# Performance work log

Hardware: AMD Instinct MI355X
Metric: run time of the kernel (lower is better)

Reference implementation:

```python
import jax, jax.numpy as jnp
import numpy as np

H, D, R, S, K, EV = 8, 256, 6, 2, 2, 2   # num_heads, head_dim, ratio, shared_head, topk, expand_v
HID = 2048
DV = D * EV            # head_v_dim = 512
KEY_DIM = H * D        # 2048
VAL_DIM = KEY_DIM * EV # 4096


def setup_inputs() -> dict:
    key = jax.random.key(0)
    ks = jax.random.split(key, 9)
    b, t = 2, 1024
    def lin(k, fan_in, shape):
        # ~torch default linear init scale
        return jax.random.normal(k, shape, jnp.float32) * (fan_in ** -0.5)
    return {
        "hidden_states": jax.random.normal(ks[0], (b, t, HID), jnp.float32),
        "Wq": lin(ks[1], HID, (HID, KEY_DIM)),
        "Wk": lin(ks[2], HID, (HID, KEY_DIM)),
        "Wv": lin(ks[3], HID, (HID, VAL_DIM)),
        "Wq_exp": lin(ks[4], D, (H, D, D * R)),  # per-head q expert expansion (ModuleList -> batched)
        "Wk_exp": lin(ks[5], D, (H, D, D * R)),
        "Wgate": lin(ks[6], D, (D, R - S)),
        "Wg": lin(ks[7], HID, (HID, VAL_DIM)),
        "Wo": lin(ks[8], VAL_DIM, (VAL_DIM, HID)),
    }


def reference(hidden_states, Wq, Wk, Wv, Wq_exp, Wk_exp, Wgate, Wg, Wo):
    b, t, _ = hidden_states.shape
    # base projections, split into heads: [H, b, t, D]
    q = (hidden_states @ Wq).reshape(b, t, H, D).transpose(2, 0, 1, 3)
    k = (hidden_states @ Wk).reshape(b, t, H, D).transpose(2, 0, 1, 3)
    v = (hidden_states @ Wv).reshape(b, t, H, DV)  # [b, t, H, DV]

    # --- sparse routing on q (gate over ratio - shared experts) ---
    logits = jnp.einsum('hbtd,dn->hbtn', q, Wgate)
    scores = jax.nn.softmax(logits.astype(jnp.float32), axis=-1)
    w, idx = jax.lax.top_k(scores, K)
    w = w / jnp.sum(w, axis=-1, keepdims=True)
    idx = idx + S  # shift past shared experts
    # scatter top-k weights into full [H, b, t, R]
    full = jnp.sum(jax.nn.one_hot(idx, R, dtype=w.dtype) * w[..., None], axis=-2)
    full = full.at[..., :S].set(1.0 / S)
    full = full / jnp.sum(full, axis=-1, keepdims=True)
    rw = full.astype(hidden_states.dtype).transpose(3, 1, 2, 0)  # [R, b, t, H]
    mask = (rw != 0).astype(hidden_states.dtype)                 # [R, b, t, H]

    # --- per-head expert expansions: [R, b, t, H, D] ---
    qe = jnp.einsum('hbtd,hde->hbte', q, Wq_exp).reshape(H, b, t, R, D).transpose(3, 1, 2, 0, 4)
    ke = jnp.einsum('hbtd,hde->hbte', k, Wk_exp).reshape(H, b, t, R, D).transpose(3, 1, 2, 0, 4)
    ve = jnp.broadcast_to(v[None], (R, b, t, H, DV))
    qe = qe * mask[..., None]
    ke = ke * mask[..., None]
    ve = ve * mask[..., None]

    # --- dense attention per (expert, batch, head) ---
    attn = jax.nn.softmax(jnp.einsum('rbqhd,rbkhd->rbhqk', qe, ke) / (D ** 0.5), axis=-1)
    o = jnp.einsum('rbhqk,rbkhd->rbqhd', attn, ve)  # [R, b, t, H, DV]

    # --- weighted combine over experts + gated output ---
    o = jnp.einsum('rbthd,rbth->bthd', o, rw)
    g = (hidden_states @ Wg).reshape(b, t, H, DV)
    o = o * jax.nn.silu(g)
    return o.reshape(b, t, VAL_DIM) @ Wo
```

## Files before the change

### kernel.cpp

```cpp
#include <hip/hip_runtime.h>
#include <hip/hip_bf16.h>
#include <cstdint>
#include <cstddef>

typedef __bf16 bf16_t;
typedef __bf16 bf16x8 __attribute__((ext_vector_type(8)));
typedef float f32x4 __attribute__((ext_vector_type(4)));

typedef __attribute__((address_space(3))) unsigned int lds_uint_t;
typedef __attribute__((address_space(1))) unsigned int glob_uint_t;

__device__ __forceinline__ void gload16(const void* g, void* l) {
  __builtin_amdgcn_global_load_lds((const glob_uint_t*)g, (lds_uint_t*)l, 16, 0, 0);
}

__device__ __forceinline__ f32x4 mfma16(bf16x8 a, bf16x8 b, f32x4 c) {
  return __builtin_amdgcn_mfma_f32_16x16x32_bf16(a, b, c, 0, 0, 0);
}

__global__ __launch_bounds__(256) void conv_bf16_k(const float* __restrict__ in,
                                                   bf16_t* __restrict__ out, int n8) {
  int i = blockIdx.x * 256 + threadIdx.x;
  if (i >= n8) return;
  f32x4 a = *(const f32x4*)(in + (size_t)i * 8);
  f32x4 b = *(const f32x4*)(in + (size_t)i * 8 + 4);
  bf16x8 o;
  o[0] = (bf16_t)a[0]; o[1] = (bf16_t)a[1]; o[2] = (bf16_t)a[2]; o[3] = (bf16_t)a[3];
  o[4] = (bf16_t)b[0]; o[5] = (bf16_t)b[1]; o[6] = (bf16_t)b[2]; o[7] = (bf16_t)b[3];
  *(bf16x8*)(out + (size_t)i * 8) = o;
}

__global__ __launch_bounds__(256) void tconv_k(const float* __restrict__ in, bf16_t* __restrict__ out,
                                               int R, int C, size_t inZ, size_t outZ) {
  __shared__ __align__(16) bf16_t t[64 * 72];
  in += (size_t)blockIdx.z * inZ;
  out += (size_t)blockIdx.z * outZ;
  const int c0 = blockIdx.x * 64, r0 = blockIdx.y * 64;
  const int tid = threadIdx.x;
#pragma unroll
  for (int it = 0; it < 4; it++) {
    int c = tid + it * 256;
    int row = c >> 4, ch = c & 15;
    f32x4 v = *(const f32x4*)(in + (size_t)(r0 + row) * C + c0 + ch * 4);
#pragma unroll
    for (int j = 0; j < 4; j++) t[(ch * 4 + j) * 72 + row] = (bf16_t)v[j];
  }
  __syncthreads();
#pragma unroll
  for (int it = 0; it < 2; it++) {
    int c = tid + it * 256;
    int oc = c >> 3, ch = c & 7;
    bf16x8 v = *(const bf16x8*)(t + oc * 72 + ch * 8);
    *(bf16x8*)(out + (size_t)(c0 + oc) * R + r0 + ch * 8) = v;
  }
}

__global__ __launch_bounds__(256) void tv_k(const bf16_t* __restrict__ v, bf16_t* __restrict__ Vt) {
  __shared__ __align__(16) bf16_t t[64 * 72];
  const int tt0 = blockIdx.x * 64;
  const int dv0 = blockIdx.y * 64;
  const int bh = blockIdx.z;
  const int b = bh >> 3, h = bh & 7;
  const int tid = threadIdx.x;
  const bf16_t* src = v + (size_t)(b * 1024 + tt0) * 12288 + 8192 + h * 512 + dv0;
#pragma unroll
  for (int it = 0; it < 2; it++) {
    int c = tid + it * 256;
    int row = c >> 3, ch = c & 7;
    bf16x8 x = *(const bf16x8*)(src + (size_t)row * 12288 + ch * 8);
#pragma unroll
    for (int j = 0; j < 8; j++) t[(ch * 8 + j) * 72 + row] = x[j];
  }
  __syncthreads();
  bf16_t* dst = Vt + (size_t)bh * 524288 + (size_t)dv0 * 1024 + tt0;
#pragma unroll
  for (int it = 0; it < 2; it++) {
    int c = tid + it * 256;
    int od = c >> 3, ch = c & 7;
    bf16x8 x = *(const bf16x8*)(t + od * 72 + ch * 8);
    *(bf16x8*)(dst + (size_t)od * 1024 + ch * 8) = x;
  }
}

__global__ __launch_bounds__(256) void wfuse_k(const float* __restrict__ Wq, const float* __restrict__ Wgate,
                                               float* __restrict__ Wf) {
  __shared__ float wg[1024];
  const int tid = threadIdx.x;
  for (int i = tid; i < 1024; i += 256) wg[i] = Wgate[i];
  __syncthreads();
  const int kk = blockIdx.x * 64 + (tid & 63);
  const int oid = tid >> 6;
  float acc[8] = {0, 0, 0, 0, 0, 0, 0, 0};
  const float* wr = Wq + (size_t)kk * 2048;
#pragma unroll
  for (int half = 0; half < 2; half++) {
    const int h = oid * 2 + half;
    const float* seg = wr + h * 256;
    for (int d = 0; d < 256; d += 4) {
      f32x4 q4 = *(const f32x4*)(seg + d);
#pragma unroll
      for (int n = 0; n < 4; n++) {
        acc[half * 4 + n] += q4[0] * wg[(d + 0) * 4 + n] + q4[1] * wg[(d + 1) * 4 + n] +
                             q4[2] * wg[(d + 2) * 4 + n] + q4[3] * wg[(d + 3) * 4 + n];
      }
    }
  }
#pragma unroll
  for (int jj = 0; jj < 8; jj++) Wf[(size_t)kk * 32 + oid * 8 + jj] = acc[jj];
}

__global__ __launch_bounds__(256) void logits_k(const float* __restrict__ hs, const float* __restrict__ Wf,
                                                float* __restrict__ lg) {
  __shared__ __align__(16) float hrow[2048];
  __shared__ float red[8][32];
  const int bt = blockIdx.x;
  const int tid = threadIdx.x;
  const float* src = hs + (size_t)bt * 2048;
  for (int i = tid; i < 512; i += 256) *(f32x4*)&hrow[i * 4] = *(const f32x4*)(src + i * 4);
  __syncthreads();
  const int j = tid & 31, part = tid >> 5;
  float acc = 0.f;
  for (int kk = part * 256; kk < part * 256 + 256; kk++) acc += hrow[kk] * Wf[(size_t)kk * 32 + j];
  red[part][j] = acc;
  __syncthreads();
  if (tid < 32) {
    float s = 0.f;
#pragma unroll
    for (int p = 0; p < 8; p++) s += red[p][tid];
    lg[(size_t)bt * 32 + tid] = s;
  }
}

__global__ __launch_bounds__(256) void routing_k(const float* __restrict__ lg, float* __restrict__ rw) {
  int gid = blockIdx.x * 256 + threadIdx.x;
  if (gid >= 16384) return;
  const int h = gid >> 11;
  const int bt = gid & 2047;
  const int b = bt >> 10, tt = bt & 1023;
  f32x4 l = *(const f32x4*)(lg + (size_t)bt * 32 + h * 4);
  float mx = fmaxf(fmaxf(l[0], l[1]), fmaxf(l[2], l[3]));
  float e0 = __expf(l[0] - mx), e1 = __expf(l[1] - mx), e2 = __expf(l[2] - mx), e3 = __expf(l[3] - mx);
  float den = e0 + e1 + e2 + e3;
  float s[4] = {e0 / den, e1 / den, e2 / den, e3 / den};
  int i1 = 0;
#pragma unroll
  for (int i = 1; i < 4; i++) if (s[i] > s[i1]) i1 = i;
  int i2 = (i1 == 0) ? 1 : 0;
#pragma unroll
  for (int i = 0; i < 4; i++) if (i != i1 && s[i] > s[i2]) i2 = i;
  float sw = s[i1] + s[i2];
  float w1 = s[i1] / sw, w2 = s[i2] / sw;
  float tot = 1.0f + w1 + w2;
  float o[6] = {0.5f / tot, 0.5f / tot, 0.f, 0.f, 0.f, 0.f};
  o[2 + i1] = w1 / tot;
  o[2 + i2] = w2 / tot;
#pragma unroll
  for (int r = 0; r < 6; r++) rw[(size_t)((r * 2 + b) * 8 + h) * 1024 + tt] = o[r];
}

template <int MODE>
__global__ __launch_bounds__(256) void gemm_bt(const bf16_t* __restrict__ A, const bf16_t* __restrict__ B,
                                               void* __restrict__ Cp, int K, int lda, int ldb, int ldc) {
  __shared__ __align__(16) bf16_t lsA[128 * 64];
  __shared__ __align__(16) bf16_t lsB[128 * 64];
  const int tid = threadIdx.x;
  const int lane = tid & 63, wv = tid >> 6;
  const int lrow = lane & 15, lgrp = lane >> 4;
  const int wr = wv >> 1, wc = wv & 1;
  const int bn = blockIdx.x * 128, bm = blockIdx.y * 128;

  f32x4 zero = {0.f, 0.f, 0.f, 0.f};
  f32x4 acc[4][4];
#pragma unroll
  for (int i = 0; i < 4; i++)
#pragma unroll
    for (int j = 0; j < 4; j++) acc[i][j] = zero;

  for (int k0 = 0; k0 < K; k0 += 64) {
    __syncthreads();
#pragma unroll
    for (int it = 0; it < 4; it++) {
      int c = tid + it * 256;
      int row = c >> 3, coff = (c & 7) * 16;
      gload16((const char*)A + ((size_t)(bm + row) * lda + k0) * 2 + coff, (char*)lsA + row * 128 + coff);
      gload16((const char*)B + ((size_t)(bn + row) * ldb + k0) * 2 + coff, (char*)lsB + row * 128 + coff);
    }
    __syncthreads();
#pragma unroll
    for (int kk = 0; kk < 2; kk++) {
      bf16x8 af[4], bfr[4];
#pragma unroll
      for (int m4 = 0; m4 < 4; m4++)
        af[m4] = *(const bf16x8*)((const char*)lsA + (wr * 64 + m4 * 16 + lrow) * 128 + kk * 64 + lgrp * 16);
#pragma unroll
      for (int n4 = 0; n4 < 4; n4++)
        bfr[n4] = *(const bf16x8*)((const char*)lsB + (wc * 64 + n4 * 16 + lrow) * 128 + kk * 64 + lgrp * 16);
#pragma unroll
      for (int m4 = 0; m4 < 4; m4++)
#pragma unroll
        for (int n4 = 0; n4 < 4; n4++) acc[m4][n4] = mfma16(af[m4], bfr[n4], acc[m4][n4]);
    }
  }
#pragma unroll
  for (int m4 = 0; m4 < 4; m4++) {
#pragma unroll
    for (int i = 0; i < 4; i++) {
      const int row = bm + wr * 64 + m4 * 16 + lgrp * 4 + i;
#pragma unroll
      for (int n4 = 0; n4 < 4; n4++) {
        const int col = bn + wc * 64 + n4 * 16 + lrow;
        float v = acc[m4][n4][i];
        if constexpr (MODE == 0) {
          ((bf16_t*)Cp)[(size_t)row * ldc + col] = (bf16_t)v;
        } else {
          ((float*)Cp)[(size_t)row * ldc + col] = v;
        }
      }
    }
  }
}

__global__ __launch_bounds__(256) void gemm_exp(const bf16_t* __restrict__ qkg, const bf16_t* __restrict__ Wqe,
                                                const bf16_t* __restrict__ Wke, bf16_t* __restrict__ qeB,
                                                bf16_t* __restrict__ keB) {
  __shared__ __align__(16) bf16_t lsA[128 * 64];
  __shared__ __align__(16) bf16_t lsB[128 * 64];
  const int tid = threadIdx.x;
  const int lane = tid & 63, wv = tid >> 6;
  const int lrow = lane & 15, lgrp = lane >> 4;
  const int wr = wv >> 1, wc = wv & 1;
  const int bn = blockIdx.x * 128, bm = blockIdx.y * 128;
  const int z = blockIdx.z;
  const int sel = z >> 3, hh = z & 7;
  const bf16_t* A = qkg + sel * 2048 + hh * 256;
  const bf16_t* B = (sel ? Wke : Wqe) + (size_t)hh * 393216;
  bf16_t* C = sel ? keB : qeB;

  f32x4 zero = {0.f, 0.f, 0.f, 0.f};
  f32x4 acc[4][4];
#pragma unroll
  for (int i = 0; i < 4; i++)
#pragma unroll
    for (int j = 0; j < 4; j++) acc[i][j] = zero;

  for (int k0 = 0; k0 < 256; k0 += 64) {
    __syncthreads();
#pragma unroll
    for (int it = 0; it < 4; it++) {
      int c = tid + it * 256;
      int row = c >> 3, coff = (c & 7) * 16;
      gload16((const char*)A + ((size_t)(bm + row) * 12288 + k0) * 2 + coff, (char*)lsA + row * 128 + coff);
      gload16((const char*)B + ((size_t)(bn + row) * 256 + k0) * 2 + coff, (char*)lsB + row * 128 + coff);
    }
    __syncthreads();
#pragma unroll
    for (int kk = 0; kk < 2; kk++) {
      bf16x8 af[4], bfr[4];
#pragma unroll
      for (int m4 = 0; m4 < 4; m4++)
        af[m4] = *(const bf16x8*)((const char*)lsA + (wr * 64 + m4 * 16 + lrow) * 128 + kk * 64 + lgrp * 16);
#pragma unroll
      for (int n4 = 0; n4 < 4; n4++)
        bfr[n4] = *(const bf16x8*)((const char*)lsB + (wc * 64 + n4 * 16 + lrow) * 128 + kk * 64 + lgrp * 16);
#pragma unroll
      for (int m4 = 0; m4 < 4; m4++)
#pragma unroll
        for (int n4 = 0; n4 < 4; n4++) acc[m4][n4] = mfma16(af[m4], bfr[n4], acc[m4][n4]);
    }
  }
#pragma unroll
  for (int m4 = 0; m4 < 4; m4++) {
#pragma unroll
    for (int i = 0; i < 4; i++) {
      const int row = bm + wr * 64 + m4 * 16 + lgrp * 4 + i;
      const int bb = row >> 10, tt = row & 1023;
#pragma unroll
      for (int n4 = 0; n4 < 4; n4++) {
        const int col = bn + wc * 64 + n4 * 16 + lrow;
        const int rr = col >> 8, dd = col & 255;
        C[((size_t)((rr * 2 + bb) * 8 + hh) * 1024 + tt) * 256 + dd] = (bf16_t)acc[m4][n4][i];
      }
    }
  }
}

__global__ __launch_bounds__(256, 2) void attn_k(const bf16_t* __restrict__ qe, const bf16_t* __restrict__ ke,
                                                 const bf16_t* __restrict__ Vt, const float* __restrict__ rw,
                                                 const bf16_t* __restrict__ g, bf16_t* __restrict__ oc) {
  __shared__ __align__(16) bf16_t ldsK[2][32 * 256];
  __shared__ __align__(16) bf16_t ldsV[2][256 * 32];
  __shared__ __align__(16) bf16_t ldsP[4 * 16 * 40];

  const int f = (blockIdx.x & 7) * 64 + (blockIdx.x >> 3);
  const int qt = f & 15, dvh = (f >> 4) & 1, bh = f >> 5;

  const int tid = threadIdx.x;
  const int wv = tid >> 6, lane = tid & 63;
  const int lrow = lane & 15, lgrp = lane >> 4;
  const int b = bh >> 3, h = bh & 7;
  const int qw = qt * 64 + wv * 16;

  const char* vbase = (const char*)Vt + ((size_t)bh * 524288 + (size_t)dvh * 262144) * 2;

  auto issue_tile = [&](int rr, int kt, int buf) {
    const char* kb = (const char*)ke + ((size_t)((rr * 2 + b) * 8 + h) * 262144 + (size_t)kt * 8192) * 2;
    char* lk = (char*)ldsK[buf];
#pragma unroll
    for (int it = 0; it < 4; it++) {
      int p = (wv * 4 + it) * 1024 + (lane << 4);
      int row = p >> 9, off = p & 511;
      gload16(kb + (size_t)row * 512 + (off ^ ((row & 7) << 4)), lk + p);
    }
    const char* vb = vbase + kt * 64;
    char* lv = (char*)ldsV[buf];
#pragma unroll
    for (int it = 0; it < 4; it++) {
      int p = (wv * 4 + it) * 1024 + (lane << 4);
      int row = p >> 6, off = p & 63;
      gload16(vb + (size_t)row * 2048 + (off ^ (((row >> 1) & 3) << 4)), lv + p);
    }
  };

  f32x4 zero = {0.f, 0.f, 0.f, 0.f};
  f32x4 Otot[16];
#pragma unroll
  for (int n = 0; n < 16; n++) Otot[n] = zero;

  int cur = 0;
  issue_tile(0, 0, 0);

  for (int r = 0; r < 6; r++) {
    const size_t rbh = (size_t)((r * 2 + b) * 8 + h);
    const bf16_t* qbase = qe + rbh * 262144;
    const float* rwb = rw + rbh * 1024;

    bf16x8 qf[8];
#pragma unroll
    for (int c = 0; c < 8; c++)
      qf[c] = *(const bf16x8*)(qbase + (size_t)(qw + lrow) * 256 + c * 32 + lgrp * 8);
    float rwq[4];
#pragma unroll
    for (int i = 0; i < 4; i++) rwq[i] = rwb[qw + lgrp * 4 + i];

    float Lp[4] = {0.f, 0.f, 0.f, 0.f};
    f32x4 accO[16];
#pragma unroll
    for (int n = 0; n < 16; n++) accO[n] = zero;

    for (int kt = 0; kt < 32; kt++) {
      asm volatile("s_waitcnt vmcnt(0) lgkmcnt(0)" ::: "memory");
      __syncthreads();
      {
        int nr = r + ((kt == 31) ? 1 : 0);
        int nkt = (kt + 1) & 31;
        if (nr < 6) issue_tile(nr, nkt, cur ^ 1);
      }
      const char* lK = (const char*)ldsK[cur];
      const char* lV = (const char*)ldsV[cur];
      const float* rwk = rwb + kt * 32;
      float mk0 = rwk[lrow], mk1 = rwk[16 + lrow];

      f32x4 sac0 = zero, sac1 = zero;
      __builtin_amdgcn_s_setprio(1);
#pragma unroll
      for (int c = 0; c < 8; c++) {
        int col = (c * 64 + lgrp * 16) ^ ((lrow & 7) << 4);
        bf16x8 k0 = *(const bf16x8*)(lK + (size_t)lrow * 512 + col);
        bf16x8 k1 = *(const bf16x8*)(lK + (size_t)(16 + lrow) * 512 + col);
        sac0 = mfma16(qf[c], k0, sac0);
        sac1 = mfma16(qf[c], k1, sac1);
      }
      __builtin_amdgcn_s_setprio(0);
      bf16_t* pb = ldsP + wv * 640;
#pragma unroll
      for (int i = 0; i < 4; i++) {
        float e0 = __expf(sac0[i] * 0.0625f);
        float e1 = __expf(sac1[i] * 0.0625f);
        pb[(i * 4 + lgrp) * 40 + lrow] = (bf16_t)((mk0 != 0.f) ? e0 : 0.f);
        pb[(i * 4 + lgrp) * 40 + 16 + lrow] = (bf16_t)((mk1 != 0.f) ? e1 : 0.f);
        Lp[i] += ((mk0 != 0.f) ? e0 : 1.f) + ((mk1 != 0.f) ? e1 : 1.f);
      }
      bf16x8 pa = *(const bf16x8*)(pb + ((lrow & 3) * 4 + (lrow >> 2)) * 40 + lgrp * 8);
      __builtin_amdgcn_s_setprio(1);
#pragma unroll
      for (int n = 0; n < 16; n++) {
        int row = n * 16 + lrow;
        int col = (lgrp * 16) ^ (((row >> 1) & 3) << 4);
        bf16x8 vf = *(const bf16x8*)(lV + (size_t)row * 64 + col);
        accO[n] = mfma16(pa, vf, accO[n]);
      }
      __builtin_amdgcn_s_setprio(0);
      cur ^= 1;
    }
#pragma unroll
    for (int i = 0; i < 4; i++) {
      float v = Lp[i];
      v += __shfl_xor(v, 1, 16);
      v += __shfl_xor(v, 2, 16);
      v += __shfl_xor(v, 4, 16);
      v += __shfl_xor(v, 8, 16);
      float inv = rwq[i] / v;
#pragma unroll
      for (int n = 0; n < 16; n++) Otot[n][i] += accO[n][i] * inv;
    }
  }

#pragma unroll
  for (int i = 0; i < 4; i++) {
    const size_t grow = ((size_t)(b * 1024 + qw + lgrp * 4 + i)) * 12288 + 4096 + h * 512 + dvh * 256;
    const size_t orow = ((size_t)(b * 1024 + qw + lgrp * 4 + i)) * 4096 + h * 512 + dvh * 256;
#pragma unroll
    for (int n = 0; n < 16; n++) {
      float gv = (float)g[grow + n * 16 + lrow];
      float sg = gv / (1.f + __expf(-gv));
      oc[orow + n * 16 + lrow] = (bf16_t)(Otot[n][i] * sg);
    }
  }
}

extern "C" void kernel_launch(void* const* d_in, const int* in_sizes, int n_in,
                              void* d_out, int out_size, void* d_ws, size_t ws_size,
                              hipStream_t stream) {
  const float* hs  = (const float*)d_in[0];
  const float* Wq  = (const float*)d_in[1];
  const float* Wk  = (const float*)d_in[2];
  const float* Wv  = (const float*)d_in[3];
  const float* Wqe = (const float*)d_in[4];
  const float* Wke = (const float*)d_in[5];
  const float* Wgt = (const float*)d_in[6];
  const float* Wg  = (const float*)d_in[7];
  const float* Wo  = (const float*)d_in[8];
  float* out = (float*)d_out;

  const size_t MB = 1024 * 1024;
  char* w = (char*)d_ws;
  bf16_t* hs_bf = (bf16_t*)(w + 0 * MB);
  bf16_t* WcatT = (bf16_t*)(w + 8 * MB);
  bf16_t* qeB   = (bf16_t*)(w + 0 * MB);
  bf16_t* WoT   = (bf16_t*)(w + 56 * MB);
  bf16_t* WqeT  = (bf16_t*)(w + 72 * MB);
  bf16_t* WkeT  = (bf16_t*)(w + 78 * MB);
  bf16_t* qkg   = (bf16_t*)(w + 84 * MB);
  bf16_t* Vt    = (bf16_t*)(w + 132 * MB);
  bf16_t* keB   = (bf16_t*)(w + 148 * MB);
  bf16_t* ocB   = (bf16_t*)(w + 196 * MB);
  float*  Wf    = (float*)(w + 212 * MB);
  float*  lg    = (float*)(w + 212 * MB + 262144);
  float*  rwB   = (float*)(w + 212 * MB + 524288);
  (void)ws_size; (void)in_sizes; (void)n_in; (void)out_size;

  conv_bf16_k<<<2048, 256, 0, stream>>>(hs, hs_bf, 524288);
  tconv_k<<<dim3(32, 32, 1), 256, 0, stream>>>(Wq, WcatT, 2048, 2048, 0, 0);
  tconv_k<<<dim3(32, 32, 1), 256, 0, stream>>>(Wk, WcatT + 2048 * 2048, 2048, 2048, 0, 0);
  tconv_k<<<dim3(64, 32, 1), 256, 0, stream>>>(Wg, WcatT + 4096 * 2048, 2048, 4096, 0, 0);
  tconv_k<<<dim3(64, 32, 1), 256, 0, stream>>>(Wv, WcatT + 8192 * 2048, 2048, 4096, 0, 0);
  tconv_k<<<dim3(32, 64, 1), 256, 0, stream>>>(Wo, WoT, 4096, 2048, 0, 0);
  tconv_k<<<dim3(24, 4, 8), 256, 0, stream>>>(Wqe, WqeT, 256, 1536, 393216, 393216);
  tconv_k<<<dim3(24, 4, 8), 256, 0, stream>>>(Wke, WkeT, 256, 1536, 393216, 393216);

  wfuse_k<<<32, 256, 0, stream>>>(Wq, Wgt, Wf);
  logits_k<<<2048, 256, 0, stream>>>(hs, Wf, lg);
  routing_k<<<64, 256, 0, stream>>>(lg, rwB);

  gemm_bt<0><<<dim3(96, 16, 1), 256, 0, stream>>>(hs_bf, WcatT, qkg, 2048, 2048, 2048, 12288);
  tv_k<<<dim3(16, 8, 16), 256, 0, stream>>>(qkg, Vt);

  gemm_exp<<<dim3(12, 16, 16), 256, 0, stream>>>(qkg, WqeT, WkeT, qeB, keB);

  attn_k<<<512, 256, 0, stream>>>(qeB, keB, Vt, rwB, qkg, ocB);

  gemm_bt<2><<<dim3(16, 16, 1), 256, 0, stream>>>(ocB, WoT, out, 4096, 4096, 4096, 2048);
}
```

Measured before the change: 723.3 us.

## Shrink attention blocks to two waves, single-buffer tiles, add N64 output GEMM

The attention kernel moves from 4-wave blocks over 64 queries to 2-wave blocks over 32 queries, launching twice as many blocks. It also drops K/V double buffering in favour of a single LDS buffer with synchronous load, wait and sync on every tile. The output projection now uses a new 128x64-tile GEMM instead of the 128x128 one, giving more blocks for better CU coverage. The costs are more K/V reloads from global memory per query, no overlap of loads with MFMA work, and an extra barrier per iteration.

```diff
diff --git a/kernel.cpp b/kernel.cpp
--- a/kernel.cpp
+++ b/kernel.cpp
@@ -220,6 +220,65 @@
   }
 }
 
+__global__ __launch_bounds__(256) void gemm_n64(const bf16_t* __restrict__ A, const bf16_t* __restrict__ B,
+                                                float* __restrict__ C, int K, int lda, int ldb, int ldc) {
+  __shared__ __align__(16) bf16_t lsA[128 * 64];
+  __shared__ __align__(16) bf16_t lsB[64 * 64];
+  const int tid = threadIdx.x;
+  const int lane = tid & 63, wr = tid >> 6;
+  const int lrow = lane & 15, lgrp = lane >> 4;
+  const int bn = blockIdx.x * 64, bm = blockIdx.y * 128;
+
+  f32x4 zero = {0.f, 0.f, 0.f, 0.f};
+  f32x4 acc[2][4];
+#pragma unroll
+  for (int i = 0; i < 2; i++)
+#pragma unroll
+    for (int j = 0; j < 4; j++) acc[i][j] = zero;
+
+  for (int k0 = 0; k0 < K; k0 += 64) {
+    __syncthreads();
+#pragma unroll
+    for (int it = 0; it < 4; it++) {
+      int c = tid + it * 256;
+      int row = c >> 3, coff = (c & 7) * 16;
+      gload16((const char*)A + ((size_t)(bm + row) * lda + k0) * 2 + coff, (char*)lsA + row * 128 + coff);
+    }
+#pragma unroll
+    for (int it = 0; it < 2; it++) {
+      int c = tid + it * 256;
+      int row = c >> 3, coff = (c & 7) * 16;
+      gload16((const char*)B + ((size_t)(bn + row) * ldb + k0) * 2 + coff, (char*)lsB + row * 128 + coff);
+    }
+    __syncthreads();
+#pragma unroll
+    for (int kk = 0; kk < 2; kk++) {
+      bf16x8 af[2], bfr[4];
+#pragma unroll
+      for (int m2 = 0; m2 < 2; m2++)
+        af[m2] = *(const bf16x8*)((const char*)lsA + (wr * 32 + m2 * 16 + lrow) * 128 + kk * 64 + lgrp * 16);
+#pragma unroll
+      for (int n4 = 0; n4 < 4; n4++)
+        bfr[n4] = *(const bf16x8*)((const char*)lsB + (n4 * 16 + lrow) * 128 + kk * 64 + lgrp * 16);
+#pragma unroll
+      for (int m2 = 0; m2 < 2; m2++)
+#pragma unroll
+        for (int n4 = 0; n4 < 4; n4++) acc[m2][n4] = mfma16(af[m2], bfr[n4], acc[m2][n4]);
+    }
+  }
+#pragma unroll
+  for (int m2 = 0; m2 < 2; m2++) {
+#pragma unroll
+    for (int i = 0; i < 4; i++) {
+      const int row = bm + wr * 32 + m2 * 16 + lgrp * 4 + i;
+#pragma unroll
+      for (int n4 = 0; n4 < 4; n4++) {
+        C[(size_t)row * ldc + bn + n4 * 16 + lrow] = acc[m2][n4][i];
+      }
+    }
+  }
+}
+
 __global__ __launch_bounds__(256) void gemm_exp(const bf16_t* __restrict__ qkg, const bf16_t* __restrict__ Wqe,
                                                 const bf16_t* __restrict__ Wke, bf16_t* __restrict__ qeB,
                                                 bf16_t* __restrict__ keB) {
@@ -284,38 +343,38 @@
   }
 }
 
-__global__ __launch_bounds__(256, 2) void attn_k(const bf16_t* __restrict__ qe, const bf16_t* __restrict__ ke,
+__global__ __launch_bounds__(128, 2) void attn_k(const bf16_t* __restrict__ qe, const bf16_t* __restrict__ ke,
                                                  const bf16_t* __restrict__ Vt, const float* __restrict__ rw,
                                                  const bf16_t* __restrict__ g, bf16_t* __restrict__ oc) {
-  __shared__ __align__(16) bf16_t ldsK[2][32 * 256];
-  __shared__ __align__(16) bf16_t ldsV[2][256 * 32];
-  __shared__ __align__(16) bf16_t ldsP[4 * 16 * 40];
-
-  const int f = (blockIdx.x & 7) * 64 + (blockIdx.x >> 3);
-  const int qt = f & 15, dvh = (f >> 4) & 1, bh = f >> 5;
+  __shared__ __align__(16) bf16_t ldsK[32 * 256];
+  __shared__ __align__(16) bf16_t ldsV[256 * 32];
+  __shared__ __align__(16) bf16_t ldsP[2 * 16 * 40];
+
+  const int f = (blockIdx.x & 7) * 128 + (blockIdx.x >> 3);
+  const int dvh = f & 1, qt = (f >> 1) & 31, bh = f >> 6;
 
   const int tid = threadIdx.x;
   const int wv = tid >> 6, lane = tid & 63;
   const int lrow = lane & 15, lgrp = lane >> 4;
   const int b = bh >> 3, h = bh & 7;
-  const int qw = qt * 64 + wv * 16;
+  const int qw = qt * 32 + wv * 16;
 
   const char* vbase = (const char*)Vt + ((size_t)bh * 524288 + (size_t)dvh * 262144) * 2;
 
-  auto issue_tile = [&](int rr, int kt, int buf) {
+  auto issue_tile = [&](int rr, int kt) {
     const char* kb = (const char*)ke + ((size_t)((rr * 2 + b) * 8 + h) * 262144 + (size_t)kt * 8192) * 2;
-    char* lk = (char*)ldsK[buf];
-#pragma unroll
-    for (int it = 0; it < 4; it++) {
-      int p = (wv * 4 + it) * 1024 + (lane << 4);
+    char* lk = (char*)ldsK;
+#pragma unroll
+    for (int it = 0; it < 8; it++) {
+      int p = it * 2048 + tid * 16;
       int row = p >> 9, off = p & 511;
       gload16(kb + (size_t)row * 512 + (off ^ ((row & 7) << 4)), lk + p);
     }
     const char* vb = vbase + kt * 64;
-    char* lv = (char*)ldsV[buf];
-#pragma unroll
-    for (int it = 0; it < 4; it++) {
-      int p = (wv * 4 + it) * 1024 + (lane << 4);
+    char* lv = (char*)ldsV;
+#pragma unroll
+    for (int it = 0; it < 8; it++) {
+      int p = it * 2048 + tid * 16;
       int row = p >> 6, off = p & 63;
       gload16(vb + (size_t)row * 2048 + (off ^ (((row >> 1) & 3) << 4)), lv + p);
     }
@@ -325,9 +384,6 @@
   f32x4 Otot[16];
 #pragma unroll
   for (int n = 0; n < 16; n++) Otot[n] = zero;
-
-  int cur = 0;
-  issue_tile(0, 0, 0);
 
   for (int r = 0; r < 6; r++) {
     const size_t rbh = (size_t)((r * 2 + b) * 8 + h);
@@ -348,15 +404,12 @@
     for (int n = 0; n < 16; n++) accO[n] = zero;
 
     for (int kt = 0; kt < 32; kt++) {
+      issue_tile(r, kt);
       asm volatile("s_waitcnt vmcnt(0) lgkmcnt(0)" ::: "memory");
       __syncthreads();
-      {
-        int nr = r + ((kt == 31) ? 1 : 0);
-        int nkt = (kt + 1) & 31;
-        if (nr < 6) issue_tile(nr, nkt, cur ^ 1);
-      }
-      const char* lK = (const char*)ldsK[cur];
-      const char* lV = (const char*)ldsV[cur];
+
+      const char* lK = (const char*)ldsK;
+      const char* lV = (const char*)ldsV;
       const float* rwk = rwb + kt * 32;
       float mk0 = rwk[lrow], mk1 = rwk[16 + lrow];
 
@@ -390,7 +443,7 @@
         accO[n] = mfma16(pa, vf, accO[n]);
       }
       __builtin_amdgcn_s_setprio(0);
-      cur ^= 1;
+      __syncthreads();
     }
 #pragma unroll
     for (int i = 0; i < 4; i++) {
@@ -467,7 +520,7 @@
 
   gemm_exp<<<dim3(12, 16, 16), 256, 0, stream>>>(qkg, WqeT, WkeT, qeB, keB);
 
-  attn_k<<<512, 256, 0, stream>>>(qeB, keB, Vt, rwB, qkg, ocB);
-
-  gemm_bt<2><<<dim3(16, 16, 1), 256, 0, stream>>>(ocB, WoT, out, 4096, 4096, 4096, 2048);
-}
+  attn_k<<<1024, 128, 0, stream>>>(qeB, keB, Vt, rwB, qkg, ocB);
+
+  gemm_n64<<<dim3(32, 16, 1), 256, 0, stream>>>(ocB, WoT, out, 4096, 4096, 4096, 2048);
+}
```

Measured after the change: 763.0 us. 1.05x slower.
